# Optimization experiments

Hardware: AMD Instinct MI355X
Metric: run time of the kernel (lower is better)

The kernel has to match this reference:

```python
import jax, jax.numpy as jnp
import numpy as np

B, T, C, H = 4, 2048, 1024, 16
HS = C // H  # head size = 64

def setup_inputs() -> dict:
    key = jax.random.key(0)
    ks = jax.random.split(key, 3)
    x = jax.random.normal(ks[0], (B, T, C), dtype=jnp.float32)
    w_attn = jax.random.normal(ks[1], (C, 3 * C), dtype=jnp.float32) * (1.0 / np.sqrt(C))
    b_attn = jnp.zeros((3 * C,), dtype=jnp.float32)
    w_proj = jax.random.normal(ks[2], (C, C), dtype=jnp.float32) * (1.0 / np.sqrt(C))
    b_proj = jnp.zeros((C,), dtype=jnp.float32)
    return {"x": x, "w_attn": w_attn, "b_attn": b_attn, "w_proj": w_proj, "b_proj": b_proj}

def reference(x, w_attn, b_attn, w_proj, b_proj):
    b, t, c = x.shape
    qkv = x @ w_attn + b_attn                       # [B,T,3C]
    q, k, v = jnp.split(qkv, 3, axis=2)             # each [B,T,C]
    # [B,T,C] -> [B,H,T,HS]
    q = q.reshape(b, t, H, HS).transpose(0, 2, 1, 3)
    k = k.reshape(b, t, H, HS).transpose(0, 2, 1, 3)
    v = v.reshape(b, t, H, HS).transpose(0, 2, 1, 3)
    scale = 1.0 / np.sqrt(HS)
    att = jnp.einsum('bhqd,bhkd->bhqk', q, k) * scale   # [B,H,T,T]
    causal = jnp.tril(jnp.ones((t, t), dtype=bool))
    att = jnp.where(causal[None, None, :, :], att, -jnp.inf)
    att = jax.nn.softmax(att, axis=-1)
    y = jnp.einsum('bhqk,bhkd->bhqd', att, v)           # [B,H,T,HS]
    y = y.transpose(0, 2, 1, 3).reshape(b, t, c)        # [B,T,C]
    return y @ w_proj + b_proj
```

## Files before the change

### kernel.cpp

```cpp
#include <hip/hip_runtime.h>
#include <hip/hip_bf16.h>

#define B_ 4
#define T_ 2048
#define C_ 1024
#define H_ 16
#define HS_ 64
#define M_ (B_*T_)
#define QSCALE 0.18033688011112042f

typedef __bf16 bf16_t;
typedef bf16_t bf16x8 __attribute__((ext_vector_type(8)));
typedef float f32x4 __attribute__((ext_vector_type(4)));
typedef unsigned short ushort_t;

__device__ __forceinline__ unsigned short f2bf(float f) {
    __hip_bfloat16 h = __float2bfloat16(f);
    return __builtin_bit_cast(unsigned short, h);
}

__device__ __forceinline__ void glds16(const void* g, void* l) {
    __builtin_amdgcn_global_load_lds((const __attribute__((address_space(1))) void*)g,
                                     (__attribute__((address_space(3))) void*)l, 16, 0, 0);
}

__launch_bounds__(256)
__global__ void cvt_x(const float* __restrict__ in, ushort_t* __restrict__ out) {
    int i = blockIdx.x * 256 + threadIdx.x;
    const float4* p = (const float4*)in;
    float4 a = p[i * 2], b = p[i * 2 + 1];
    ushort4 o0, o1;
    o0.x = f2bf(a.x); o0.y = f2bf(a.y); o0.z = f2bf(a.z); o0.w = f2bf(a.w);
    o1.x = f2bf(b.x); o1.y = f2bf(b.y); o1.z = f2bf(b.z); o1.w = f2bf(b.w);
    *(ushort4*)&out[i * 8] = o0;
    *(ushort4*)&out[i * 8 + 4] = o1;
}

__launch_bounds__(256)
__global__ void transpose_cvt(const float* __restrict__ w, ushort_t* __restrict__ wT,
                              int K, int N) {
    __shared__ ushort_t Ts[64][72];
    const int n0 = blockIdx.x * 64, k0 = blockIdx.y * 64;
    const int t = threadIdx.x, r = t >> 2, cq = t & 3;
    #pragma unroll
    for (int j = 0; j < 4; j++) {
        float4 v = *(const float4*)&w[(size_t)(k0 + r) * N + n0 + cq * 16 + j * 4];
        ushort4 o;
        o.x = f2bf(v.x); o.y = f2bf(v.y); o.z = f2bf(v.z); o.w = f2bf(v.w);
        *(ushort4*)&Ts[r][cq * 16 + j * 4] = o;
    }
    __syncthreads();
    #pragma unroll
    for (int j = 0; j < 4; j++) {
        ushort4 o;
        o.x = Ts[cq * 16 + j * 4 + 0][r];
        o.y = Ts[cq * 16 + j * 4 + 1][r];
        o.z = Ts[cq * 16 + j * 4 + 2][r];
        o.w = Ts[cq * 16 + j * 4 + 3][r];
        *(ushort4*)&wT[(size_t)(n0 + r) * K + k0 + cq * 16 + j * 4] = o;
    }
}

__launch_bounds__(256)
__global__ void qkv_gemm(const ushort_t* __restrict__ xb, const ushort_t* __restrict__ wT,
                         const float* __restrict__ bias,
                         ushort_t* __restrict__ qw, ushort_t* __restrict__ kw,
                         ushort_t* __restrict__ vt) {
    const int K = C_;
    __shared__ ushort_t As[128 * 64];
    __shared__ ushort_t Bs[128 * 64];
    const int tid = threadIdx.x, lane = tid & 63, wid = tid >> 6;
    const int cl = lane & 15, gl = lane >> 4;
    const int waveM = wid >> 1, waveN = wid & 1;
    const int m0 = blockIdx.y * 128, n0 = blockIdx.x * 128;
    const int srow = tid >> 3, scq = tid & 7;

    f32x4 acc[4][4];
    #pragma unroll
    for (int mf = 0; mf < 4; mf++)
        #pragma unroll
        for (int nf = 0; nf < 4; nf++) acc[mf][nf] = (f32x4)0.0f;

    for (int kk = 0; kk < K; kk += 64) {
        #pragma unroll
        for (int i = 0; i < 4; i++) {
            int row = srow + i * 32;
            glds16(&xb[(size_t)(m0 + row) * K + kk + scq * 8], &As[row * 64 + scq * 8]);
            glds16(&wT[(size_t)(n0 + row) * K + kk + scq * 8], &Bs[row * 64 + scq * 8]);
        }
        __syncthreads();
        bf16x8 a[2][4], b[2][4];
        #pragma unroll
        for (int ks = 0; ks < 2; ks++) {
            #pragma unroll
            for (int mf = 0; mf < 4; mf++)
                a[ks][mf] = *(bf16x8*)&As[(waveM * 64 + mf * 16 + cl) * 64 + ks * 32 + gl * 8];
            #pragma unroll
            for (int nf = 0; nf < 4; nf++)
                b[ks][nf] = *(bf16x8*)&Bs[(waveN * 64 + nf * 16 + cl) * 64 + ks * 32 + gl * 8];
        }
        #pragma unroll
        for (int ks = 0; ks < 2; ks++)
            #pragma unroll
            for (int mf = 0; mf < 4; mf++)
                #pragma unroll
                for (int nf = 0; nf < 4; nf++)
                    acc[mf][nf] = __builtin_amdgcn_mfma_f32_16x16x32_bf16(a[ks][mf], b[ks][nf], acc[mf][nf], 0, 0, 0);
        __syncthreads();
    }
    const int secb = n0 >> 10;
    #pragma unroll
    for (int mf = 0; mf < 4; mf++)
        #pragma unroll
        for (int nf = 0; nf < 4; nf++)
            #pragma unroll
            for (int r = 0; r < 4; r++) {
                int rg = m0 + waveM * 64 + mf * 16 + 4 * gl + r;
                int cg = n0 + waveN * 64 + nf * 16 + cl;
                float val = acc[mf][nf][r] + bias[cg];
                int cc = cg & 1023;
                int h = cc >> 6, hs = cc & 63;
                int bb = rg >> 11, tq = rg & 2047;
                if (secb == 0)
                    qw[(((size_t)(bb * H_ + h)) * T_ + tq) * HS_ + hs] = f2bf(val * QSCALE);
                else if (secb == 1)
                    kw[(((size_t)(bb * H_ + h)) * T_ + tq) * HS_ + hs] = f2bf(val);
                else
                    vt[(((size_t)(bb * H_ + h)) * HS_ + hs) * T_ + tq] = f2bf(val);
            }
}

__launch_bounds__(512, 4)
__global__ void attn_mfma(const ushort_t* __restrict__ qw,
                          const ushort_t* __restrict__ kw,
                          const ushort_t* __restrict__ vt,
                          ushort_t* __restrict__ yw) {
    __shared__ ushort_t Ks[128][72];
    __shared__ ushort_t Vts[64][136];
    __shared__ ushort_t Ps[8][16][136];
    const int tid = threadIdx.x, lane = tid & 63, wid = tid >> 6;
    const int cl = lane & 15, gl = lane >> 4;
    const int qp = blockIdx.x;
    const int bh = blockIdx.y;
    const size_t base = (size_t)bh * T_ * HS_;
    const int bq = bh >> 4, h = bh & 15;
    const int srow = tid >> 3, scq = tid & 7;

    for (int half = 0; half < 2; half++) {
        const int qt = half ? (15 - qp) : qp;
        const int q0 = qt * 128 + wid * 16;
        const int ntiles = qt + 1;

        bf16x8 qf[2];
        #pragma unroll
        for (int kh = 0; kh < 2; kh++)
            qf[kh] = *(const bf16x8*)&qw[base + (size_t)(q0 + cl) * HS_ + kh * 32 + 8 * gl];

        f32x4 o_acc[4];
        #pragma unroll
        for (int dn = 0; dn < 4; dn++) o_acc[dn] = (f32x4)0.0f;
        float m_ = -INFINITY, l_ = 0.f;

        bf16x8 kpre[2], vpre[2], knew[2], vnew[2];
        kpre[0] = *(const bf16x8*)&kw[base + (size_t)srow * HS_ + scq * 8];
        kpre[1] = *(const bf16x8*)&kw[base + (size_t)(64 + srow) * HS_ + scq * 8];
        vpre[0] = *(const bf16x8*)&vt[base + (size_t)srow * T_ + scq * 8];
        vpre[1] = *(const bf16x8*)&vt[base + (size_t)srow * T_ + 64 + scq * 8];

        for (int kt = 0; kt < ntiles; kt++) {
            __syncthreads();
            if (kt + 1 < ntiles) {
                knew[0] = *(const bf16x8*)&kw[base + (size_t)((kt + 1) * 128 + srow) * HS_ + scq * 8];
                knew[1] = *(const bf16x8*)&kw[base + (size_t)((kt + 1) * 128 + 64 + srow) * HS_ + scq * 8];
                vnew[0] = *(const bf16x8*)&vt[base + (size_t)srow * T_ + (kt + 1) * 128 + scq * 8];
                vnew[1] = *(const bf16x8*)&vt[base + (size_t)srow * T_ + (kt + 1) * 128 + 64 + scq * 8];
            }
            *(bf16x8*)&Ks[srow][scq * 8] = kpre[0];
            *(bf16x8*)&Ks[64 + srow][scq * 8] = kpre[1];
            *(bf16x8*)&Vts[srow][scq * 8] = vpre[0];
            *(bf16x8*)&Vts[srow][scq * 8 + 64] = vpre[1];
            __syncthreads();

            {
                const bool full = (kt * 128 + 127 <= q0);

                f32x4 st[8];
                #pragma unroll
                for (int kn = 0; kn < 8; kn++) {
                    bf16x8 kf0 = *(bf16x8*)&Ks[kn * 16 + cl][8 * gl];
                    bf16x8 kf1 = *(bf16x8*)&Ks[kn * 16 + cl][32 + 8 * gl];
                    f32x4 t0 = (f32x4)0.0f;
                    t0 = __builtin_amdgcn_mfma_f32_16x16x32_bf16(kf0, qf[0], t0, 0, 0, 0);
                    st[kn] = __builtin_amdgcn_mfma_f32_16x16x32_bf16(kf1, qf[1], t0, 0, 0, 0);
                }
                if (!full) {
                    const int qg = q0 + cl;
                    #pragma unroll
                    for (int kn = 0; kn < 8; kn++)
                        #pragma unroll
                        for (int r = 0; r < 4; r++) {
                            int kv = kt * 128 + kn * 16 + 4 * gl + r;
                            if (kv > qg) st[kn][r] = -INFINITY;
                        }
                }

                float pmax = st[0][0];
                #pragma unroll
                for (int kn = 0; kn < 8; kn++)
                    #pragma unroll
                    for (int r = 0; r < 4; r++) pmax = fmaxf(pmax, st[kn][r]);
                if (!__all(pmax <= m_ + 8.0f)) {
                    float mx = pmax;
                    mx = fmaxf(mx, __shfl_xor(mx, 16));
                    mx = fmaxf(mx, __shfl_xor(mx, 32));
                    float nm = fmaxf(m_, mx);
                    float al = exp2f(m_ - nm);
                    l_ *= al;
                    #pragma unroll
                    for (int r = 0; r < 4; r++) {
                        float ag = __shfl(al, 4 * gl + r);
                        #pragma unroll
                        for (int dn = 0; dn < 4; dn++) o_acc[dn][r] *= ag;
                    }
                    m_ = nm;
                }

                float ps = 0.f;
                #pragma unroll
                for (int kn = 0; kn < 8; kn++) {
                    float p0 = exp2f(st[kn][0] - m_);
                    float p1 = exp2f(st[kn][1] - m_);
                    float p2 = exp2f(st[kn][2] - m_);
                    float p3 = exp2f(st[kn][3] - m_);
                    ps += (p0 + p1) + (p2 + p3);
                    unsigned lo, hi;
                    asm("v_cvt_pk_bf16_f32 %0, %1, %2" : "=v"(lo) : "v"(p0), "v"(p1));
                    asm("v_cvt_pk_bf16_f32 %0, %1, %2" : "=v"(hi) : "v"(p2), "v"(p3));
                    uint2 wv; wv.x = lo; wv.y = hi;
                    *(uint2*)&Ps[wid][cl][kn * 16 + 4 * gl] = wv;
                }
                l_ += ps;

                bf16x8 pf[4];
                #pragma unroll
                for (int ks = 0; ks < 4; ks++)
                    pf[ks] = *(bf16x8*)&Ps[wid][cl][ks * 32 + 8 * gl];
                #pragma unroll
                for (int dn = 0; dn < 4; dn++)
                    #pragma unroll
                    for (int ks = 0; ks < 4; ks++) {
                        bf16x8 vf = *(bf16x8*)&Vts[dn * 16 + cl][ks * 32 + 8 * gl];
                        o_acc[dn] = __builtin_amdgcn_mfma_f32_16x16x32_bf16(pf[ks], vf, o_acc[dn], 0, 0, 0);
                    }
            }
            #pragma unroll
            for (int i = 0; i < 2; i++) { kpre[i] = knew[i]; vpre[i] = vnew[i]; }
        }

        float ls = l_;
        ls += __shfl_xor(ls, 16);
        ls += __shfl_xor(ls, 32);
        float linv = 1.0f / ls;
        #pragma unroll
        for (int r = 0; r < 4; r++) {
            float lr = __shfl(linv, 4 * gl + r);
            int qg = q0 + 4 * gl + r;
            #pragma unroll
            for (int dn = 0; dn < 4; dn++) {
                int d = dn * 16 + cl;
                yw[((size_t)(bq * T_ + qg)) * C_ + h * HS_ + d] = f2bf(o_acc[dn][r] * lr);
            }
        }
    }
}

__launch_bounds__(256)
__global__ void proj_gemm(const ushort_t* __restrict__ y, const ushort_t* __restrict__ wT,
                          const float* __restrict__ bias, float* __restrict__ out) {
    const int K = C_, N = C_;
    __shared__ ushort_t As[128 * 64];
    __shared__ ushort_t Bs[128 * 64];
    const int tid = threadIdx.x, lane = tid & 63, wid = tid >> 6;
    const int cl = lane & 15, gl = lane >> 4;
    const int waveM = wid >> 1, waveN = wid & 1;
    const int m0 = blockIdx.y * 128, n0 = blockIdx.x * 128;
    const int srow = tid >> 3, scq = tid & 7;

    f32x4 acc[4][4];
    #pragma unroll
    for (int mf = 0; mf < 4; mf++)
        #pragma unroll
        for (int nf = 0; nf < 4; nf++) acc[mf][nf] = (f32x4)0.0f;

    for (int kk = 0; kk < K; kk += 64) {
        #pragma unroll
        for (int i = 0; i < 4; i++) {
            int row = srow + i * 32;
            glds16(&y[(size_t)(m0 + row) * K + kk + scq * 8], &As[row * 64 + scq * 8]);
            glds16(&wT[(size_t)(n0 + row) * K + kk + scq * 8], &Bs[row * 64 + scq * 8]);
        }
        __syncthreads();
        bf16x8 a[2][4], b[2][4];
        #pragma unroll
        for (int ks = 0; ks < 2; ks++) {
            #pragma unroll
            for (int mf = 0; mf < 4; mf++)
                a[ks][mf] = *(bf16x8*)&As[(waveM * 64 + mf * 16 + cl) * 64 + ks * 32 + gl * 8];
            #pragma unroll
            for (int nf = 0; nf < 4; nf++)
                b[ks][nf] = *(bf16x8*)&Bs[(waveN * 64 + nf * 16 + cl) * 64 + ks * 32 + gl * 8];
        }
        #pragma unroll
        for (int ks = 0; ks < 2; ks++)
            #pragma unroll
            for (int mf = 0; mf < 4; mf++)
                #pragma unroll
                for (int nf = 0; nf < 4; nf++)
                    acc[mf][nf] = __builtin_amdgcn_mfma_f32_16x16x32_bf16(a[ks][mf], b[ks][nf], acc[mf][nf], 0, 0, 0);
        __syncthreads();
    }
    #pragma unroll
    for (int mf = 0; mf < 4; mf++)
        #pragma unroll
        for (int nf = 0; nf < 4; nf++)
            #pragma unroll
            for (int r = 0; r < 4; r++) {
                int rg = m0 + waveM * 64 + mf * 16 + 4 * gl + r;
                int cg = n0 + waveN * 64 + nf * 16 + cl;
                out[(size_t)rg * N + cg] = acc[mf][nf][r] + bias[cg];
            }
}

extern "C" void kernel_launch(void* const* d_in, const int* in_sizes, int n_in,
                              void* d_out, int out_size, void* d_ws, size_t ws_size,
                              hipStream_t stream) {
    const float* x      = (const float*)d_in[0];
    const float* w_attn = (const float*)d_in[1];
    const float* b_attn = (const float*)d_in[2];
    const float* w_proj = (const float*)d_in[3];
    const float* b_proj = (const float*)d_in[4];
    float* out = (float*)d_out;

    const size_t E = (size_t)M_ * C_;
    ushort_t* qw  = (ushort_t*)d_ws;
    ushort_t* kw  = qw + E;
    ushort_t* vt  = kw + E;
    ushort_t* xy  = vt + E;
    ushort_t* wat = xy + E;
    ushort_t* wpt = vt;

    cvt_x<<<dim3(4096), 256, 0, stream>>>(x, xy);
    transpose_cvt<<<dim3(48, 16), 256, 0, stream>>>(w_attn, wat, C_, 3 * C_);
    qkv_gemm<<<dim3(24, 64), 256, 0, stream>>>(xy, wat, b_attn, qw, kw, vt);
    attn_mfma<<<dim3(8, 64), 512, 0, stream>>>(qw, kw, vt, xy);
    transpose_cvt<<<dim3(16, 16), 256, 0, stream>>>(w_proj, wpt, C_, C_);
    proj_gemm<<<dim3(8, 64), 256, 0, stream>>>(xy, wpt, b_proj, out);
}
```

Measured before the change: 307.9 us.

## Double-buffer GEMM LDS tiles with K=32 steps and XOR-swizzled layout

Both the QKV and projection GEMMs now use two LDS buffers of 128x32 tiles, prefetching the next K slice with global_load_lds while MFMAs run on the current one, which drops one barrier per iteration. The global source column is XOR-swizzled on load and un-swizzled on the LDS fragment read to cut bank conflicts. The tradeoff is twice as many loop iterations with a shorter K step, which means less MFMA work per barrier.

Measured after the change: 297.7 us. 3.3% less time.

```diff
diff --git a/kernel.cpp b/kernel.cpp
--- a/kernel.cpp
+++ b/kernel.cpp
@@ -67,13 +67,15 @@
                          ushort_t* __restrict__ qw, ushort_t* __restrict__ kw,
                          ushort_t* __restrict__ vt) {
     const int K = C_;
-    __shared__ ushort_t As[128 * 64];
-    __shared__ ushort_t Bs[128 * 64];
+    __shared__ ushort_t As[2][128 * 32];
+    __shared__ ushort_t Bs[2][128 * 32];
     const int tid = threadIdx.x, lane = tid & 63, wid = tid >> 6;
     const int cl = lane & 15, gl = lane >> 4;
     const int waveM = wid >> 1, waveN = wid & 1;
     const int m0 = blockIdx.y * 128, n0 = blockIdx.x * 128;
-    const int srow = tid >> 3, scq = tid & 7;
+    const int srow = tid >> 2, scq = tid & 3;
+    const int gsw = scq ^ ((srow >> 1) & 3);
+    const int asw = 8 * (gl ^ ((cl >> 1) & 3));
 
     f32x4 acc[4][4];
     #pragma unroll
@@ -81,32 +83,38 @@
         #pragma unroll
         for (int nf = 0; nf < 4; nf++) acc[mf][nf] = (f32x4)0.0f;
 
-    for (int kk = 0; kk < K; kk += 64) {
-        #pragma unroll
-        for (int i = 0; i < 4; i++) {
-            int row = srow + i * 32;
-            glds16(&xb[(size_t)(m0 + row) * K + kk + scq * 8], &As[row * 64 + scq * 8]);
-            glds16(&wT[(size_t)(n0 + row) * K + kk + scq * 8], &Bs[row * 64 + scq * 8]);
+    #pragma unroll
+    for (int i = 0; i < 2; i++) {
+        int row = srow + i * 64;
+        glds16(&xb[(size_t)(m0 + row) * K + gsw * 8], &As[0][row * 32 + scq * 8]);
+        glds16(&wT[(size_t)(n0 + row) * K + gsw * 8], &Bs[0][row * 32 + scq * 8]);
+    }
+    __syncthreads();
+
+    int cur = 0;
+    for (int kk = 0; kk < K; kk += 32) {
+        if (kk + 32 < K) {
+            #pragma unroll
+            for (int i = 0; i < 2; i++) {
+                int row = srow + i * 64;
+                glds16(&xb[(size_t)(m0 + row) * K + kk + 32 + gsw * 8], &As[cur ^ 1][row * 32 + scq * 8]);
+                glds16(&wT[(size_t)(n0 + row) * K + kk + 32 + gsw * 8], &Bs[cur ^ 1][row * 32 + scq * 8]);
+            }
         }
+        bf16x8 a[4], b[4];
+        #pragma unroll
+        for (int mf = 0; mf < 4; mf++)
+            a[mf] = *(bf16x8*)&As[cur][(waveM * 64 + mf * 16 + cl) * 32 + asw];
+        #pragma unroll
+        for (int nf = 0; nf < 4; nf++)
+            b[nf] = *(bf16x8*)&Bs[cur][(waveN * 64 + nf * 16 + cl) * 32 + asw];
+        #pragma unroll
+        for (int mf = 0; mf < 4; mf++)
+            #pragma unroll
+            for (int nf = 0; nf < 4; nf++)
+                acc[mf][nf] = __builtin_amdgcn_mfma_f32_16x16x32_bf16(a[mf], b[nf], acc[mf][nf], 0, 0, 0);
         __syncthreads();
-        bf16x8 a[2][4], b[2][4];
-        #pragma unroll
-        for (int ks = 0; ks < 2; ks++) {
-            #pragma unroll
-            for (int mf = 0; mf < 4; mf++)
-                a[ks][mf] = *(bf16x8*)&As[(waveM * 64 + mf * 16 + cl) * 64 + ks * 32 + gl * 8];
-            #pragma unroll
-            for (int nf = 0; nf < 4; nf++)
-                b[ks][nf] = *(bf16x8*)&Bs[(waveN * 64 + nf * 16 + cl) * 64 + ks * 32 + gl * 8];
-        }
-        #pragma unroll
-        for (int ks = 0; ks < 2; ks++)
-            #pragma unroll
-            for (int mf = 0; mf < 4; mf++)
-                #pragma unroll
-                for (int nf = 0; nf < 4; nf++)
-                    acc[mf][nf] = __builtin_amdgcn_mfma_f32_16x16x32_bf16(a[ks][mf], b[ks][nf], acc[mf][nf], 0, 0, 0);
-        __syncthreads();
+        cur ^= 1;
     }
     const int secb = n0 >> 10;
     #pragma unroll
@@ -278,13 +286,15 @@
 __global__ void proj_gemm(const ushort_t* __restrict__ y, const ushort_t* __restrict__ wT,
                           const float* __restrict__ bias, float* __restrict__ out) {
     const int K = C_, N = C_;
-    __shared__ ushort_t As[128 * 64];
-    __shared__ ushort_t Bs[128 * 64];
+    __shared__ ushort_t As[2][128 * 32];
+    __shared__ ushort_t Bs[2][128 * 32];
     const int tid = threadIdx.x, lane = tid & 63, wid = tid >> 6;
     const int cl = lane & 15, gl = lane >> 4;
     const int waveM = wid >> 1, waveN = wid & 1;
     const int m0 = blockIdx.y * 128, n0 = blockIdx.x * 128;
-    const int srow = tid >> 3, scq = tid & 7;
+    const int srow = tid >> 2, scq = tid & 3;
+    const int gsw = scq ^ ((srow >> 1) & 3);
+    const int asw = 8 * (gl ^ ((cl >> 1) & 3));
 
     f32x4 acc[4][4];
     #pragma unroll
@@ -292,32 +302,38 @@
         #pragma unroll
         for (int nf = 0; nf < 4; nf++) acc[mf][nf] = (f32x4)0.0f;
 
-    for (int kk = 0; kk < K; kk += 64) {
-        #pragma unroll
-        for (int i = 0; i < 4; i++) {
-            int row = srow + i * 32;
-            glds16(&y[(size_t)(m0 + row) * K + kk + scq * 8], &As[row * 64 + scq * 8]);
-            glds16(&wT[(size_t)(n0 + row) * K + kk + scq * 8], &Bs[row * 64 + scq * 8]);
+    #pragma unroll
+    for (int i = 0; i < 2; i++) {
+        int row = srow + i * 64;
+        glds16(&y[(size_t)(m0 + row) * K + gsw * 8], &As[0][row * 32 + scq * 8]);
+        glds16(&wT[(size_t)(n0 + row) * K + gsw * 8], &Bs[0][row * 32 + scq * 8]);
+    }
+    __syncthreads();
+
+    int cur = 0;
+    for (int kk = 0; kk < K; kk += 32) {
+        if (kk + 32 < K) {
+            #pragma unroll
+            for (int i = 0; i < 2; i++) {
+                int row = srow + i * 64;
+                glds16(&y[(size_t)(m0 + row) * K + kk + 32 + gsw * 8], &As[cur ^ 1][row * 32 + scq * 8]);
+                glds16(&wT[(size_t)(n0 + row) * K + kk + 32 + gsw * 8], &Bs[cur ^ 1][row * 32 + scq * 8]);
+            }
         }
+        bf16x8 a[4], b[4];
+        #pragma unroll
+        for (int mf = 0; mf < 4; mf++)
+            a[mf] = *(bf16x8*)&As[cur][(waveM * 64 + mf * 16 + cl) * 32 + asw];
+        #pragma unroll
+        for (int nf = 0; nf < 4; nf++)
+            b[nf] = *(bf16x8*)&Bs[cur][(waveN * 64 + nf * 16 + cl) * 32 + asw];
+        #pragma unroll
+        for (int mf = 0; mf < 4; mf++)
+            #pragma unroll
+            for (int nf = 0; nf < 4; nf++)
+                acc[mf][nf] = __builtin_amdgcn_mfma_f32_16x16x32_bf16(a[mf], b[nf], acc[mf][nf], 0, 0, 0);
         __syncthreads();
-        bf16x8 a[2][4], b[2][4];
-        #pragma unroll
-        for (int ks = 0; ks < 2; ks++) {
-            #pragma unroll
-            for (int mf = 0; mf < 4; mf++)
-                a[ks][mf] = *(bf16x8*)&As[(waveM * 64 + mf * 16 + cl) * 64 + ks * 32 + gl * 8];
-            #pragma unroll
-            for (int nf = 0; nf < 4; nf++)
-                b[ks][nf] = *(bf16x8*)&Bs[(waveN * 64 + nf * 16 + cl) * 64 + ks * 32 + gl * 8];
-        }
-        #pragma unroll
-        for (int ks = 0; ks < 2; ks++)
-            #pragma unroll
-            for (int mf = 0; mf < 4; mf++)
-                #pragma unroll
-                for (int nf = 0; nf < 4; nf++)
-                    acc[mf][nf] = __builtin_amdgcn_mfma_f32_16x16x32_bf16(a[ks][mf], b[ks][nf], acc[mf][nf], 0, 0, 0);
-        __syncthreads();
+        cur ^= 1;
     }
     #pragma unroll
     for (int mf = 0; mf < 4; mf++)
```

## Double-buffer GEMM LDS tiles with XOR swizzle, block remap, and MFMA priority

Applied to the files above, without the earlier changes.

Both GEMM kernels now double-buffer their A/B tiles in LDS, prefetching the next k-tile with global_load_lds while the current tile feeds MFMA. This replaces two barriers per iteration with one. Global-side XOR swizzling of the 16-byte column slots is meant to remove LDS bank conflicts on fragment reads. Blocks are remapped from a 1D grid so that groups of blocks share tiles in L2. s_setprio is raised around the MFMA sections in the GEMMs and the attention kernel. The cost is double the LDS per block, which may lower occupancy. The proj weight transpose moves to its own workspace region and launches earlier.

Measured after the change: 293.9 us. -4.6%, faster.

```diff
diff --git a/kernel.cpp b/kernel.cpp
--- a/kernel.cpp
+++ b/kernel.cpp
@@ -67,13 +67,19 @@
                          ushort_t* __restrict__ qw, ushort_t* __restrict__ kw,
                          ushort_t* __restrict__ vt) {
     const int K = C_;
-    __shared__ ushort_t As[128 * 64];
-    __shared__ ushort_t Bs[128 * 64];
+    __shared__ ushort_t As[2][128 * 64];
+    __shared__ ushort_t Bs[2][128 * 64];
     const int tid = threadIdx.x, lane = tid & 63, wid = tid >> 6;
     const int cl = lane & 15, gl = lane >> 4;
     const int waveM = wid >> 1, waveN = wid & 1;
-    const int m0 = blockIdx.y * 128, n0 = blockIdx.x * 128;
-    const int srow = tid >> 3, scq = tid & 7;
+    const int bid = blockIdx.x;
+    const int swz = (bid & 7) * 192 + (bid >> 3);
+    const int by = swz / 24, bx = swz - by * 24;
+    const int m0 = by * 128, n0 = bx * 128;
+    const int srow = tid >> 3;
+    const int sslot = tid & 7;
+    const int gsw = sslot ^ (srow & 7);
+    const int csw = cl & 7;
 
     f32x4 acc[4][4];
     #pragma unroll
@@ -81,24 +87,37 @@
         #pragma unroll
         for (int nf = 0; nf < 4; nf++) acc[mf][nf] = (f32x4)0.0f;
 
-    for (int kk = 0; kk < K; kk += 64) {
+    auto stage = [&](int t, int b) {
+        const size_t koff = (size_t)t * 64 + gsw * 8;
         #pragma unroll
         for (int i = 0; i < 4; i++) {
-            int row = srow + i * 32;
-            glds16(&xb[(size_t)(m0 + row) * K + kk + scq * 8], &As[row * 64 + scq * 8]);
-            glds16(&wT[(size_t)(n0 + row) * K + kk + scq * 8], &Bs[row * 64 + scq * 8]);
-        }
-        __syncthreads();
+            int row = srow + 32 * i;
+            glds16(&xb[(size_t)(m0 + row) * K + koff], &As[b][row * 64 + sslot * 8]);
+            glds16(&wT[(size_t)(n0 + row) * K + koff], &Bs[b][row * 64 + sslot * 8]);
+        }
+    };
+    stage(0, 0);
+    asm volatile("s_waitcnt vmcnt(0)" ::: "memory");
+    __builtin_amdgcn_s_barrier();
+
+    int cur = 0;
+    for (int t = 0; t < 16; t++) {
+        if (t + 1 < 16) stage(t + 1, cur ^ 1);
         bf16x8 a[2][4], b[2][4];
         #pragma unroll
         for (int ks = 0; ks < 2; ks++) {
             #pragma unroll
-            for (int mf = 0; mf < 4; mf++)
-                a[ks][mf] = *(bf16x8*)&As[(waveM * 64 + mf * 16 + cl) * 64 + ks * 32 + gl * 8];
-            #pragma unroll
-            for (int nf = 0; nf < 4; nf++)
-                b[ks][nf] = *(bf16x8*)&Bs[(waveN * 64 + nf * 16 + cl) * 64 + ks * 32 + gl * 8];
-        }
+            for (int mf = 0; mf < 4; mf++) {
+                int row = waveM * 64 + mf * 16 + cl;
+                a[ks][mf] = *(bf16x8*)&As[cur][row * 64 + 8 * ((4 * ks + gl) ^ csw)];
+            }
+            #pragma unroll
+            for (int nf = 0; nf < 4; nf++) {
+                int row = waveN * 64 + nf * 16 + cl;
+                b[ks][nf] = *(bf16x8*)&Bs[cur][row * 64 + 8 * ((4 * ks + gl) ^ csw)];
+            }
+        }
+        __builtin_amdgcn_s_setprio(1);
         #pragma unroll
         for (int ks = 0; ks < 2; ks++)
             #pragma unroll
@@ -106,7 +125,12 @@
                 #pragma unroll
                 for (int nf = 0; nf < 4; nf++)
                     acc[mf][nf] = __builtin_amdgcn_mfma_f32_16x16x32_bf16(a[ks][mf], b[ks][nf], acc[mf][nf], 0, 0, 0);
-        __syncthreads();
+        __builtin_amdgcn_s_setprio(0);
+        if (t + 1 < 16) {
+            asm volatile("s_waitcnt vmcnt(0)" ::: "memory");
+            __builtin_amdgcn_s_barrier();
+            cur ^= 1;
+        }
     }
     const int secb = n0 >> 10;
     #pragma unroll
@@ -185,6 +209,7 @@
                 const bool full = (kt * 128 + 127 <= q0);
 
                 f32x4 st[8];
+                __builtin_amdgcn_s_setprio(1);
                 #pragma unroll
                 for (int kn = 0; kn < 8; kn++) {
                     bf16x8 kf0 = *(bf16x8*)&Ks[kn * 16 + cl][8 * gl];
@@ -193,6 +218,7 @@
                     t0 = __builtin_amdgcn_mfma_f32_16x16x32_bf16(kf0, qf[0], t0, 0, 0, 0);
                     st[kn] = __builtin_amdgcn_mfma_f32_16x16x32_bf16(kf1, qf[1], t0, 0, 0, 0);
                 }
+                __builtin_amdgcn_s_setprio(0);
                 if (!full) {
                     const int qg = q0 + cl;
                     #pragma unroll
@@ -245,6 +271,7 @@
                 #pragma unroll
                 for (int ks = 0; ks < 4; ks++)
                     pf[ks] = *(bf16x8*)&Ps[wid][cl][ks * 32 + 8 * gl];
+                __builtin_amdgcn_s_setprio(1);
                 #pragma unroll
                 for (int dn = 0; dn < 4; dn++)
                     #pragma unroll
@@ -252,6 +279,7 @@
                         bf16x8 vf = *(bf16x8*)&Vts[dn * 16 + cl][ks * 32 + 8 * gl];
                         o_acc[dn] = __builtin_amdgcn_mfma_f32_16x16x32_bf16(pf[ks], vf, o_acc[dn], 0, 0, 0);
                     }
+                __builtin_amdgcn_s_setprio(0);
             }
             #pragma unroll
             for (int i = 0; i < 2; i++) { kpre[i] = knew[i]; vpre[i] = vnew[i]; }
@@ -278,13 +306,19 @@
 __global__ void proj_gemm(const ushort_t* __restrict__ y, const ushort_t* __restrict__ wT,
                           const float* __restrict__ bias, float* __restrict__ out) {
     const int K = C_, N = C_;
-    __shared__ ushort_t As[128 * 64];
-    __shared__ ushort_t Bs[128 * 64];
+    __shared__ ushort_t As[2][128 * 64];
+    __shared__ ushort_t Bs[2][128 * 64];
     const int tid = threadIdx.x, lane = tid & 63, wid = tid >> 6;
     const int cl = lane & 15, gl = lane >> 4;
     const int waveM = wid >> 1, waveN = wid & 1;
-    const int m0 = blockIdx.y * 128, n0 = blockIdx.x * 128;
-    const int srow = tid >> 3, scq = tid & 7;
+    const int bid = blockIdx.x;
+    const int swz = (bid & 7) * 64 + (bid >> 3);
+    const int bx = swz & 7, by = swz >> 3;
+    const int m0 = by * 128, n0 = bx * 128;
+    const int srow = tid >> 3;
+    const int sslot = tid & 7;
+    const int gsw = sslot ^ (srow & 7);
+    const int csw = cl & 7;
 
     f32x4 acc[4][4];
     #pragma unroll
@@ -292,24 +326,37 @@
         #pragma unroll
         for (int nf = 0; nf < 4; nf++) acc[mf][nf] = (f32x4)0.0f;
 
-    for (int kk = 0; kk < K; kk += 64) {
+    auto stage = [&](int t, int b) {
+        const size_t koff = (size_t)t * 64 + gsw * 8;
         #pragma unroll
         for (int i = 0; i < 4; i++) {
-            int row = srow + i * 32;
-            glds16(&y[(size_t)(m0 + row) * K + kk + scq * 8], &As[row * 64 + scq * 8]);
-            glds16(&wT[(size_t)(n0 + row) * K + kk + scq * 8], &Bs[row * 64 + scq * 8]);
-        }
-        __syncthreads();
+            int row = srow + 32 * i;
+            glds16(&y[(size_t)(m0 + row) * K + koff],  &As[b][row * 64 + sslot * 8]);
+            glds16(&wT[(size_t)(n0 + row) * K + koff], &Bs[b][row * 64 + sslot * 8]);
+        }
+    };
+    stage(0, 0);
+    asm volatile("s_waitcnt vmcnt(0)" ::: "memory");
+    __builtin_amdgcn_s_barrier();
+
+    int cur = 0;
+    for (int t = 0; t < 16; t++) {
+        if (t + 1 < 16) stage(t + 1, cur ^ 1);
         bf16x8 a[2][4], b[2][4];
         #pragma unroll
         for (int ks = 0; ks < 2; ks++) {
             #pragma unroll
-            for (int mf = 0; mf < 4; mf++)
-                a[ks][mf] = *(bf16x8*)&As[(waveM * 64 + mf * 16 + cl) * 64 + ks * 32 + gl * 8];
-            #pragma unroll
-            for (int nf = 0; nf < 4; nf++)
-                b[ks][nf] = *(bf16x8*)&Bs[(waveN * 64 + nf * 16 + cl) * 64 + ks * 32 + gl * 8];
-        }
+            for (int mf = 0; mf < 4; mf++) {
+                int row = waveM * 64 + mf * 16 + cl;
+                a[ks][mf] = *(bf16x8*)&As[cur][row * 64 + 8 * ((4 * ks + gl) ^ csw)];
+            }
+            #pragma unroll
+            for (int nf = 0; nf < 4; nf++) {
+                int row = waveN * 64 + nf * 16 + cl;
+                b[ks][nf] = *(bf16x8*)&Bs[cur][row * 64 + 8 * ((4 * ks + gl) ^ csw)];
+            }
+        }
+        __builtin_amdgcn_s_setprio(1);
         #pragma unroll
         for (int ks = 0; ks < 2; ks++)
             #pragma unroll
@@ -317,7 +364,12 @@
                 #pragma unroll
                 for (int nf = 0; nf < 4; nf++)
                     acc[mf][nf] = __builtin_amdgcn_mfma_f32_16x16x32_bf16(a[ks][mf], b[ks][nf], acc[mf][nf], 0, 0, 0);
-        __syncthreads();
+        __builtin_amdgcn_s_setprio(0);
+        if (t + 1 < 16) {
+            asm volatile("s_waitcnt vmcnt(0)" ::: "memory");
+            __builtin_amdgcn_s_barrier();
+            cur ^= 1;
+        }
     }
     #pragma unroll
     for (int mf = 0; mf < 4; mf++)
@@ -347,12 +399,12 @@
     ushort_t* vt  = kw + E;
     ushort_t* xy  = vt + E;
     ushort_t* wat = xy + E;
-    ushort_t* wpt = vt;
+    ushort_t* wpt = wat + 3 * (size_t)C_ * C_;
 
     cvt_x<<<dim3(4096), 256, 0, stream>>>(x, xy);
     transpose_cvt<<<dim3(48, 16), 256, 0, stream>>>(w_attn, wat, C_, 3 * C_);
-    qkv_gemm<<<dim3(24, 64), 256, 0, stream>>>(xy, wat, b_attn, qw, kw, vt);
+    transpose_cvt<<<dim3(16, 16), 256, 0, stream>>>(w_proj, wpt, C_, C_);
+    qkv_gemm<<<dim3(1536), 256, 0, stream>>>(xy, wat, b_attn, qw, kw, vt);
     attn_mfma<<<dim3(8, 64), 512, 0, stream>>>(qw, kw, vt, xy);
-    transpose_cvt<<<dim3(16, 16), 256, 0, stream>>>(w_proj, wpt, C_, C_);
-    proj_gemm<<<dim3(8, 64), 256, 0, stream>>>(xy, wpt, b_proj, out);
-}
+    proj_gemm<<<dim3(512), 256, 0, stream>>>(xy, wpt, b_proj, out);
+}
```
